# Performance work log

Measured on AMD Instinct MI355X. Metric: run time of the kernel, lower is better.

The kernel has to match this reference:

```python
import jax, jax.numpy as jnp
import numpy as np

T, B, E, H = 512, 32, 512, 2048

def setup_inputs() -> dict:
    key = jax.random.key(0)
    k1, k2, k3 = jax.random.split(key, 3)
    sent = jax.random.normal(k1, (T, B, E), dtype=jnp.float32)
    lengths = jax.random.randint(k2, (B,), 1, T + 1)  # unused by the math (pack is never applied)
    # Linear(E, 3H) params (PyTorch default-ish init scale)
    W = jax.random.normal(k3, (3 * H, E), dtype=jnp.float32) * (1.0 / np.sqrt(E))
    b = jnp.zeros((3 * H,), dtype=jnp.float32)
    return {"sent": sent, "lengths": lengths, "W": W, "b": b}

def reference(sent, lengths, W, b):
    # sent: (T, B, E) time-major. Single QRNN layer, window=1, output_gate=True, zoneout=0.
    Y = jnp.einsum('tbe,he->tbh', sent, W) + b          # (T, B, 3H)
    Z, F, O = jnp.split(Y, 3, axis=-1)
    Z = jnp.tanh(Z)
    F = jax.nn.sigmoid(F)
    O = jax.nn.sigmoid(O)

    # forget-mult recurrence: c_t = f_t * z_t + (1 - f_t) * c_{t-1}, c_0 = 0
    def step(c, zf):
        z, f = zf
        c = f * z + (1.0 - f) * c
        return c, c
    c0 = jnp.zeros_like(Z[0])                            # (B, H)
    _, C = jax.lax.scan(step, c0, (Z, F))                # (T, B, H)

    Hseq = O * C                                         # QRNN output (T, B, H)
    embeds = jnp.max(Hseq, axis=0)                       # torch.max(sent_output, 0)[0] -> (B, H)
    return embeds
```

## Files before the change

kernel.cpp:

```cpp
#include <hip/hip_runtime.h>
#include <stdint.h>

#define TT 512
#define BB 32
#define EE 512
#define HH 2048

typedef __attribute__((ext_vector_type(8))) short short8;
typedef __attribute__((ext_vector_type(4))) float f32x4;

static __device__ __forceinline__ unsigned short f2bf(float f) {
    union { float f; unsigned u; } v; v.f = f;
    unsigned u = v.u;
    unsigned r = u + 0x7FFFu + ((u >> 16) & 1u);
    return (unsigned short)(r >> 16);
}

static __device__ __forceinline__ float fast_exp(float x) {
    return __builtin_amdgcn_exp2f(x * 1.44269504f);
}
static __device__ __forceinline__ float fast_rcp(float x) {
    return __builtin_amdgcn_rcpf(x);
}

__global__ void convert_inputs(const float* __restrict__ X,
                               const float* __restrict__ W,
                               unsigned short* __restrict__ Xb,
                               unsigned short* __restrict__ Wb) {
    const int nX = TT * BB * EE;
    int i = (blockIdx.x * blockDim.x + threadIdx.x) * 8;
    const float* src;
    unsigned short* dst;
    int j;
    if (i < nX) { src = X; dst = Xb; j = i; }
    else        { src = W; dst = Wb; j = i - nX; }
    float4 v0 = *(const float4*)(src + j);
    float4 v1 = *(const float4*)(src + j + 4);
    union { short8 s; unsigned short u[8]; } o;
    o.u[0] = f2bf(v0.x); o.u[1] = f2bf(v0.y); o.u[2] = f2bf(v0.z); o.u[3] = f2bf(v0.w);
    o.u[4] = f2bf(v1.x); o.u[5] = f2bf(v1.y); o.u[6] = f2bf(v1.z); o.u[7] = f2bf(v1.w);
    *(short8*)(dst + j) = o.s;
}

#define LDS_STRIDE 528

__launch_bounds__(256, 2)
__global__ void qrnn_fused(const unsigned short* __restrict__ Xb,
                           const unsigned short* __restrict__ Wb,
                           const float* __restrict__ bias,
                           float* __restrict__ out)
{
    __shared__ unsigned short lds[2][16 * LDS_STRIDE];
    __shared__ float exch[2][64][12];

    const int tid  = threadIdx.x;
    const int wv   = tid >> 6;
    const int lane = tid & 63;
    const int q    = lane >> 4;
    const int c    = lane & 15;
    const int hi   = wv >> 1;
    const int s    = wv & 1;
    const int b    = blockIdx.y;
    const int h    = blockIdx.x * 32 + hi * 16 + c;

    short8 wz[8], wf[8], wo[8];
    {
        const unsigned short* wzr = Wb + (size_t)h * EE            + s * 256;
        const unsigned short* wfr = Wb + (size_t)(HH + h) * EE     + s * 256;
        const unsigned short* wor = Wb + (size_t)(2 * HH + h) * EE + s * 256;
#pragma unroll
        for (int k = 0; k < 8; ++k) {
            int e0 = k * 32 + q * 8;
            wz[k] = *(const short8*)(wzr + e0);
            wf[k] = *(const short8*)(wfr + e0);
            wo[k] = *(const short8*)(wor + e0);
        }
    }
#pragma unroll
    for (int k = 0; k < 8; ++k) {
        asm volatile("" : "+v"(wz[k]), "+v"(wf[k]), "+v"(wo[k]));
    }

    const float b0 = (s == 0) ? bias[h]          : 0.0f;
    const float b1 = (s == 0) ? bias[HH + h]     : 0.0f;
    const float b2 = (s == 0) ? bias[2 * HH + h] : 0.0f;

    float carry = 0.0f;
    float vmax  = -1e30f;

    auto stage = [&](int ch, int buf) {
        const int row  = tid >> 4;
        const int blk0 = tid & 15;
        const unsigned short* src = Xb + ((size_t)(ch * 16 + row) * BB + b) * EE;
        unsigned short* dst = &lds[buf][row * LDS_STRIDE];
#pragma unroll
        for (int i = 0; i < 4; ++i) {
            int blk = blk0 + 16 * i;
            *(short8*)(dst + blk * 8) = *(const short8*)(src + blk * 8);
        }
    };

    stage(0, 0);
    __syncthreads();

    for (int ch = 0; ch < TT / 16; ++ch) {
        const int buf = ch & 1;
        if (ch + 1 < TT / 16) stage(ch + 1, buf ^ 1);

        f32x4 az = {b0, b0, b0, b0};
        f32x4 af = {b1, b1, b1, b1};
        f32x4 ao = {b2, b2, b2, b2};
        const unsigned short* Abase = &lds[buf][c * LDS_STRIDE + s * 256 + q * 8];
#pragma unroll
        for (int k = 0; k < 8; ++k) {
            short8 a = *(const short8*)(Abase + k * 32);
            az = __builtin_amdgcn_mfma_f32_16x16x32_bf16(a, wz[k], az, 0, 0, 0);
            af = __builtin_amdgcn_mfma_f32_16x16x32_bf16(a, wf[k], af, 0, 0, 0);
            ao = __builtin_amdgcn_mfma_f32_16x16x32_bf16(a, wo[k], ao, 0, 0, 0);
        }

        if (s == 1) {
            float* e = &exch[hi][lane][0];
            *(f32x4*)(e)     = az;
            *(f32x4*)(e + 4) = af;
            *(f32x4*)(e + 8) = ao;
        }
        __syncthreads();

        if (s == 0) {
            const float* e = &exch[hi][lane][0];
            f32x4 pz = *(const f32x4*)(e);
            f32x4 pf = *(const f32x4*)(e + 4);
            f32x4 po = *(const f32x4*)(e + 8);
            az = az + pz; af = af + pf; ao = ao + po;

            float aa[4], mm[4], oo[4];
#pragma unroll
            for (int r = 0; r < 4; ++r) {
                float e2 = fast_exp(2.0f * az[r]);
                float z  = 1.0f - 2.0f * fast_rcp(e2 + 1.0f);
                float f  = fast_rcp(1.0f + fast_exp(-af[r]));
                float o  = fast_rcp(1.0f + fast_exp(-ao[r]));
                aa[r] = f * z;
                mm[r] = 1.0f - f;
                oo[r] = o;
            }

            float A = aa[0], M = mm[0];
#pragma unroll
            for (int r = 1; r < 4; ++r) { A = aa[r] + mm[r] * A; M = mm[r] * M; }

            float Ap = __shfl_up(A, 16, 64), Mp = __shfl_up(M, 16, 64);
            if (q >= 1) { A = A + M * Ap; M = M * Mp; }
            Ap = __shfl_up(A, 32, 64); Mp = __shfl_up(M, 32, 64);
            if (q >= 2) { A = A + M * Ap; M = M * Mp; }
            float Ae = __shfl_up(A, 16, 64), Me = __shfl_up(M, 16, 64);
            if (q == 0) { Ae = 0.0f; Me = 1.0f; }
            float cc = Ae + Me * carry;

#pragma unroll
            for (int r = 0; r < 4; ++r) {
                cc = aa[r] + mm[r] * cc;
                vmax = fmaxf(vmax, oo[r] * cc);
            }

            float cend = A + M * carry;
            carry = __shfl(cend, 48 + c, 64);
        }

        __syncthreads();
    }

    if (s == 0) {
        vmax = fmaxf(vmax, __shfl_xor(vmax, 16, 64));
        vmax = fmaxf(vmax, __shfl_xor(vmax, 32, 64));
        if (q == 0) out[(size_t)b * HH + h] = vmax;
    }
}

extern "C" void kernel_launch(void* const* d_in, const int* in_sizes, int n_in,
                              void* d_out, int out_size, void* d_ws, size_t ws_size,
                              hipStream_t stream) {
    const float* sent = (const float*)d_in[0];
    const float* W    = (const float*)d_in[2];
    const float* bias = (const float*)d_in[3];
    float* out        = (float*)d_out;

    const int nX = TT * BB * EE;
    const int nW = 3 * HH * EE;
    unsigned short* Xb = (unsigned short*)d_ws;
    unsigned short* Wb = Xb + nX;

    int totalVec = (nX + nW) / 8;
    convert_inputs<<<totalVec / 256, 256, 0, stream>>>(sent, W, Xb, Wb);

    dim3 grid(HH / 32, BB);
    qrnn_fused<<<grid, 256, 0, stream>>>(Xb, Wb, bias, out);
}
```

Before: 226.9 us.

## Triple-buffer X tiles via direct global-to-LDS loads and drop one barrier per chunk

Replaces the register-staged double buffer with a three-slot LDS ring filled by global_load_lds, prefetching two chunks ahead. The partial-sum exchange buffer is double-buffered so the second per-iteration __syncthreads can be removed, and a single hand-written waitcnt+barrier per chunk waits only for the older loads. Weight fragments are pinned to AGPRs to free VGPRs. This aims to hide global load latency and cut synchronisation, at the cost of extra LDS, fragile manual vmcnt accounting, and a possible WAR hazard on the reused ring slot.

After: 235.0 us. +3.6%, slower.

```diff
diff --git a/kernel.cpp b/kernel.cpp
--- a/kernel.cpp
+++ b/kernel.cpp
@@ -8,6 +8,10 @@
 
 typedef __attribute__((ext_vector_type(8))) short short8;
 typedef __attribute__((ext_vector_type(4))) float f32x4;
+
+#define XROW 520
+#define XBUF (16 * XROW)
+#define NBUF 3
 
 static __device__ __forceinline__ unsigned short f2bf(float f) {
     union { float f; unsigned u; } v; v.f = f;
@@ -21,6 +25,13 @@
 }
 static __device__ __forceinline__ float fast_rcp(float x) {
     return __builtin_amdgcn_rcpf(x);
+}
+
+static __device__ __forceinline__ void load_lds16(const unsigned short* g, unsigned short* l) {
+    __builtin_amdgcn_global_load_lds(
+        (const __attribute__((address_space(1))) unsigned int*)(uintptr_t)g,
+        (__attribute__((address_space(3))) unsigned int*)(uintptr_t)l,
+        16, 0, 0);
 }
 
 __global__ void convert_inputs(const float* __restrict__ X,
@@ -42,16 +53,14 @@
     *(short8*)(dst + j) = o.s;
 }
 
-#define LDS_STRIDE 528
-
 __launch_bounds__(256, 2)
 __global__ void qrnn_fused(const unsigned short* __restrict__ Xb,
                            const unsigned short* __restrict__ Wb,
                            const float* __restrict__ bias,
                            float* __restrict__ out)
 {
-    __shared__ unsigned short lds[2][16 * LDS_STRIDE];
-    __shared__ float exch[2][64][12];
+    __shared__ unsigned short xlds[NBUF * XBUF];
+    __shared__ float exch[2][2][64][12];
 
     const int tid  = threadIdx.x;
     const int wv   = tid >> 6;
@@ -78,7 +87,7 @@
     }
 #pragma unroll
     for (int k = 0; k < 8; ++k) {
-        asm volatile("" : "+v"(wz[k]), "+v"(wf[k]), "+v"(wo[k]));
+        asm volatile("" : "+a"(wz[k]), "+a"(wf[k]), "+a"(wo[k]));
     }
 
     const float b0 = (s == 0) ? bias[h]          : 0.0f;
@@ -88,29 +97,29 @@
     float carry = 0.0f;
     float vmax  = -1e30f;
 
-    auto stage = [&](int ch, int buf) {
-        const int row  = tid >> 4;
-        const int blk0 = tid & 15;
-        const unsigned short* src = Xb + ((size_t)(ch * 16 + row) * BB + b) * EE;
-        unsigned short* dst = &lds[buf][row * LDS_STRIDE];
-#pragma unroll
-        for (int i = 0; i < 4; ++i) {
-            int blk = blk0 + 16 * i;
-            *(short8*)(dst + blk * 8) = *(const short8*)(src + blk * 8);
-        }
+    const unsigned short* g0 = Xb + ((size_t)(wv * 4) * BB + b) * EE + lane * 8;
+    unsigned short* l0 = &xlds[(wv * 4) * XROW];
+
+    auto stage = [&](int n, int slot) {
+        const unsigned short* g = g0 + (size_t)n * (16 * BB * EE);
+        unsigned short* l = l0 + slot * XBUF;
+#pragma unroll
+        for (int i = 0; i < 4; ++i)
+            load_lds16(g + (size_t)i * (BB * EE), l + i * XROW);
     };
 
     stage(0, 0);
-    __syncthreads();
-
-    for (int ch = 0; ch < TT / 16; ++ch) {
-        const int buf = ch & 1;
-        if (ch + 1 < TT / 16) stage(ch + 1, buf ^ 1);
+    stage(1, 1);
+    asm volatile("s_waitcnt vmcnt(4) lgkmcnt(0)\n\ts_barrier" ::: "memory");
+
+    int buf = 0;
+    for (int ch = 0; ch < 32; ++ch) {
+        if (ch < 30) stage(ch + 2, (buf + 2 >= 3) ? buf - 1 : buf + 2);
 
         f32x4 az = {b0, b0, b0, b0};
         f32x4 af = {b1, b1, b1, b1};
         f32x4 ao = {b2, b2, b2, b2};
-        const unsigned short* Abase = &lds[buf][c * LDS_STRIDE + s * 256 + q * 8];
+        const unsigned short* Abase = &xlds[buf * XBUF + c * XROW + s * 256 + q * 8];
 #pragma unroll
         for (int k = 0; k < 8; ++k) {
             short8 a = *(const short8*)(Abase + k * 32);
@@ -119,16 +128,22 @@
             ao = __builtin_amdgcn_mfma_f32_16x16x32_bf16(a, wo[k], ao, 0, 0, 0);
         }
 
+        const int eb = ch & 1;
         if (s == 1) {
-            float* e = &exch[hi][lane][0];
+            float* e = &exch[eb][hi][lane][0];
             *(f32x4*)(e)     = az;
             *(f32x4*)(e + 4) = af;
             *(f32x4*)(e + 8) = ao;
         }
-        __syncthreads();
+
+        if (ch < 30) {
+            asm volatile("s_waitcnt vmcnt(4) lgkmcnt(0)\n\ts_barrier" ::: "memory");
+        } else {
+            asm volatile("s_waitcnt vmcnt(0) lgkmcnt(0)\n\ts_barrier" ::: "memory");
+        }
 
         if (s == 0) {
-            const float* e = &exch[hi][lane][0];
+            const float* e = &exch[eb][hi][lane][0];
             f32x4 pz = *(const f32x4*)(e);
             f32x4 pf = *(const f32x4*)(e + 4);
             f32x4 po = *(const f32x4*)(e + 8);
@@ -168,7 +183,7 @@
             carry = __shfl(cend, 48 + c, 64);
         }
 
-        __syncthreads();
+        buf = (buf >= 2) ? 0 : buf + 1;
     }
 
     if (s == 0) {
```
